# Optimization experiments

Measured on AMD Instinct MI355X. Metric: run time of the kernel, lower is better.

## Reference

```python
import math
import jax, jax.numpy as jnp
import numpy as np

B, T, C, HS = 8, 2048, 1024, 64

def setup_inputs() -> dict:
    key = jax.random.key(0)
    kx, kq, kk, kv = jax.random.split(key, 4)
    x = jax.random.normal(kx, (B, T, C), dtype=jnp.float32)
    # match nn.Linear init scale roughly: U(-1/sqrt(C), 1/sqrt(C))
    lim = 1.0 / math.sqrt(C)
    Wq = jax.random.uniform(kq, (C, HS), minval=-lim, maxval=lim, dtype=jnp.float32)
    Wk = jax.random.uniform(kk, (C, HS), minval=-lim, maxval=lim, dtype=jnp.float32)
    Wv = jax.random.uniform(kv, (C, HS), minval=-lim, maxval=lim, dtype=jnp.float32)
    return {"x": x, "Wq": Wq, "Wk": Wk, "Wv": Wv}

def reference(x, Wq, Wk, Wv):
    # NOTE: original scales by 1/sqrt(hs) where hs = x.shape[-1] = embd_size,
    # not head_size. Faithfully reproduced.
    Tlen = x.shape[1]
    scale = 1.0 / math.sqrt(x.shape[-1])
    q = jnp.einsum('btc,ch->bth', x, Wq)
    k = jnp.einsum('btc,ch->bth', x, Wk)
    v = jnp.einsum('btc,ch->bth', x, Wv)
    wei = jnp.einsum('bth,bsh->bts', q, k) * scale  # [B,T,T]
    causal = jnp.tril(jnp.ones((Tlen, Tlen), dtype=bool))
    wei = jnp.where(causal, wei, -jnp.inf)
    wei = jax.nn.softmax(wei, axis=-1)
    # dropout p=0.0 -> identity
    out = jnp.einsum('bts,bsh->bth', wei, v)  # [B,T,HS]
    return out
```

## Files before the change

kernel.cpp:

```cpp
#include <hip/hip_runtime.h>
#include <hip/hip_bf16.h>


#define T_SEQ 2048
#define C_DIM 1024
#define HS 64
#define BT 16384

typedef short s8v __attribute__((ext_vector_type(8)));
typedef float f4v __attribute__((ext_vector_type(4)));

__device__ inline unsigned short f2bf(float f) {
  union { float f; unsigned u; } a; a.f = f;
  unsigned r = a.u + 0x7fffu + ((a.u >> 16) & 1u);
  return (unsigned short)(r >> 16);
}

__device__ inline unsigned pk2(float a, float b) {
  union { __hip_bfloat162 h; unsigned u; } c;
  c.h = __float22bfloat162_rn(make_float2(a, b));
  return c.u;
}

__device__ inline s8v cvt8(float4 v0, float4 v1) {
  union { unsigned u[4]; s8v v; } r;
  r.u[0] = pk2(v0.x, v0.y); r.u[1] = pk2(v0.z, v0.w);
  r.u[2] = pk2(v1.x, v1.y); r.u[3] = pk2(v1.z, v1.w);
  return r.v;
}

__device__ inline void gl_lds16(const void* g, unsigned char* lds_base,
                                unsigned uniform_byte_off) {
  __builtin_amdgcn_global_load_lds(
      (const __attribute__((address_space(1))) unsigned int*)g,
      (__attribute__((address_space(3))) unsigned int*)(lds_base + uniform_byte_off),
      16, 0, 0);
}

__global__ __launch_bounds__(256) void wt_kernel(
    const float* __restrict__ Wq, const float* __restrict__ Wk,
    const float* __restrict__ Wv, unsigned short* __restrict__ wt) {
  __shared__ float tile[64][65];
  const int bid = blockIdx.x;
  const int mat = bid >> 4, kt = bid & 15;
  const float* W = (mat == 0) ? Wq : ((mat == 1) ? Wk : Wv);
  const int t = threadIdx.x;
  const int n = t & 63, kr = t >> 6;
#pragma unroll
  for (int j = 0; j < 16; ++j) {
    const int kl = j * 4 + kr;
    tile[kl][n] = W[(kt * 64 + kl) * HS + n];
  }
  __syncthreads();
  const int n2 = t >> 2, kp = t & 3;
  unsigned int* orow =
      (unsigned int*)(wt + (size_t)(mat * 64 + n2) * C_DIM + kt * 64);
#pragma unroll
  for (int i = 0; i < 8; ++i) {
    const int k0 = kp * 16 + i * 2;
    unsigned int lo = f2bf(tile[k0][n2]);
    unsigned int hi = f2bf(tile[k0 + 1][n2]);
    orow[kp * 8 + i] = lo | (hi << 16);
  }
}

__global__ __launch_bounds__(256) void qkv_kernel(
    const float* __restrict__ x, const unsigned short* __restrict__ wt,
    unsigned short* __restrict__ qws, unsigned short* __restrict__ kws,
    unsigned short* __restrict__ vtws) {
  __shared__ unsigned char abuf[2][8192];
  __shared__ unsigned char bbuf[2][24576];

  const int tid  = threadIdx.x;
  const int wv   = tid >> 6;
  const int lane = tid & 63;
  const int m    = lane & 15;
  const int quad = lane >> 4;
  const int row0 = blockIdx.x * 32;
  const int mh   = wv >> 1;
  const int ng   = (wv & 1) * 6;

  f4v acc[6];
#pragma unroll
  for (int j = 0; j < 6; ++j) acc[j] = (f4v)0.0f;

  const unsigned au = (unsigned)__builtin_amdgcn_readfirstlane(tid & 192) << 4;

  const float* agp[2];
#pragma unroll
  for (int j = 0; j < 2; ++j) {
    const int s = tid + j * 256;
    const int r = s >> 4, p = (s & 15) ^ (r & 15);
    agp[j] = x + (size_t)(row0 + r) * C_DIM + p * 4;
  }
  const unsigned short* bgp[6];
#pragma unroll
  for (int j = 0; j < 6; ++j) {
    const int s = tid + j * 256;
    const int n = s >> 3, p = (s & 7) ^ (n & 7);
    bgp[j] = wt + (size_t)n * C_DIM + p * 8;
  }

  int aoff[2][2];
#pragma unroll
  for (int c = 0; c < 2; ++c)
#pragma unroll
    for (int t = 0; t < 2; ++t)
      aoff[c][t] = (((mh * 16 + m) * 16) + ((c * 8 + 2 * quad + t) ^ m)) << 4;
  int boff[6][2];
#pragma unroll
  for (int j = 0; j < 6; ++j) {
    const int n = (ng + j) * 16 + m;
#pragma unroll
    for (int c = 0; c < 2; ++c)
      boff[j][c] = (n * 8 + ((c * 4 + quad) ^ (n & 7))) << 4;
  }

#define STAGE(buf, kk)                                                       \
  do {                                                                       \
    _Pragma("unroll") for (int j = 0; j < 2; ++j)                            \
        gl_lds16(agp[j] + (kk), abuf[buf], au + (unsigned)(j * 4096));       \
    _Pragma("unroll") for (int j = 0; j < 6; ++j)                            \
        gl_lds16(bgp[j] + (kk), bbuf[buf], au + (unsigned)(j * 4096));       \
  } while (0)

  STAGE(0, 0);
  for (int it = 0; it < 16; ++it) {
    __syncthreads();
    if (it < 15) STAGE((it + 1) & 1, (it + 1) * 64);
    const unsigned char* aB = abuf[it & 1];
    const unsigned char* bB = bbuf[it & 1];
#pragma unroll
    for (int c = 0; c < 2; ++c) {
      float4 xa = *(const float4*)(aB + aoff[c][0]);
      float4 xb = *(const float4*)(aB + aoff[c][1]);
      s8v a = cvt8(xa, xb);
#pragma unroll
      for (int j = 0; j < 6; ++j) {
        s8v b = *(const s8v*)(bB + boff[j][c]);
        acc[j] = __builtin_amdgcn_mfma_f32_16x16x32_bf16(a, b, acc[j], 0, 0, 0);
      }
    }
  }
#undef STAGE

  const float qscale = 1.4426950408889634f / 32.0f;
#pragma unroll
  for (int j = 0; j < 6; ++j) {
    const int nt = ng + j;
    const int mat = nt >> 2, ct = nt & 3;
    const int col = ct * 16 + m;
#pragma unroll
    for (int r = 0; r < 4; ++r) {
      const int row = row0 + mh * 16 + quad * 4 + r;
      const float v = acc[j][r];
      if (mat == 0) {
        qws[row * HS + col] = f2bf(v * qscale);
      } else if (mat == 1) {
        kws[row * HS + col] = f2bf(v);
      } else {
        const int bb = row >> 11, t = row & 2047;
        const int tp = (t & ~63) | (((t & 15) << 2) | ((t >> 4) & 3));
        vtws[(bb * HS + col) * T_SEQ + tp] = f2bf(v);
      }
    }
  }
}

union __align__(16) AttnSh {
  unsigned short p[8][2][16 * 72];
  float mo[8][32][64];
};

__global__ __launch_bounds__(512) void attn_kernel(
    const unsigned short* __restrict__ qws, const unsigned short* __restrict__ kws,
    const unsigned short* __restrict__ vtws, float* __restrict__ out) {
  __shared__ AttnSh sh;
  __shared__ float ml[8][32];

  const int tid  = threadIdx.x;
  const int wv   = tid >> 6;
  const int lane = tid & 63;
  const int m    = lane & 15;
  const int quad = lane >> 4;
  const int b    = blockIdx.x & 7;
  const int qi   = (T_SEQ / 32 - 1) - (blockIdx.x >> 3);
  const int r0   = qi * 32;
  const int gr0  = b * T_SEQ + r0;

  const unsigned short* qp = qws + (size_t)(gr0 + m) * HS + quad * 8;
  s8v aqA0 = *(const s8v*)qp;
  s8v aqA1 = *(const s8v*)(qp + 32);
  s8v aqB0 = *(const s8v*)(qp + 16 * HS);
  s8v aqB1 = *(const s8v*)(qp + 16 * HS + 32);

  float liA[4] = {0.f, 0.f, 0.f, 0.f};
  float liB[4] = {0.f, 0.f, 0.f, 0.f};
  f4v oA[4], oB[4];
#pragma unroll
  for (int i = 0; i < 4; ++i) { oA[i] = (f4v)0.0f; oB[i] = (f4v)0.0f; }

  const int nst = (r0 + 32 + 63) >> 6;
  unsigned short* plA = sh.p[wv][0];
  unsigned short* plB = sh.p[wv][1];
  const int qbA = r0 + quad * 4;
  const int qbB = qbA + 16;
  const unsigned short* kbase = kws + (size_t)b * T_SEQ * HS;
  const unsigned short* vbase = vtws + (size_t)b * HS * T_SEQ;

  for (int st = wv; st < nst; st += 8) {
    const int s0 = st * 64;

    s8v kf[4][2];
#pragma unroll
    for (int ns = 0; ns < 4; ++ns) {
      const unsigned short* kp = &kbase[(size_t)(s0 + ns * 16 + m) * HS + quad * 8];
      kf[ns][0] = *(const s8v*)kp;
      kf[ns][1] = *(const s8v*)(kp + 32);
    }
    s8v vf[4][2];
#pragma unroll
    for (int hn = 0; hn < 4; ++hn) {
      const unsigned short* vp = &vbase[(size_t)(hn * 16 + m) * T_SEQ + s0 + quad * 8];
      vf[hn][0] = *(const s8v*)vp;
      vf[hn][1] = *(const s8v*)(vp + 32);
    }

    f4v sa[4], sb[4];
#pragma unroll
    for (int ns = 0; ns < 4; ++ns) {
      f4v t = (f4v)0.0f;
      t = __builtin_amdgcn_mfma_f32_16x16x32_bf16(aqA0, kf[ns][0], t, 0, 0, 0);
      t = __builtin_amdgcn_mfma_f32_16x16x32_bf16(aqA1, kf[ns][1], t, 0, 0, 0);
      sa[ns] = t;
      f4v u = (f4v)0.0f;
      u = __builtin_amdgcn_mfma_f32_16x16x32_bf16(aqB0, kf[ns][0], u, 0, 0, 0);
      u = __builtin_amdgcn_mfma_f32_16x16x32_bf16(aqB1, kf[ns][1], u, 0, 0, 0);
      sb[ns] = u;
    }

    const int sm = s0 + m;
#pragma unroll
    for (int r = 0; r < 4; ++r) {
      const int qr = qbA + r;
      const float p0 = (sm      > qr) ? 0.f : __builtin_amdgcn_exp2f(sa[0][r]);
      const float p1 = (sm + 16 > qr) ? 0.f : __builtin_amdgcn_exp2f(sa[1][r]);
      const float p2 = (sm + 32 > qr) ? 0.f : __builtin_amdgcn_exp2f(sa[2][r]);
      const float p3 = (sm + 48 > qr) ? 0.f : __builtin_amdgcn_exp2f(sa[3][r]);
      liA[r] += (p0 + p1) + (p2 + p3);
      *(uint2*)&plA[(quad * 4 + r) * 72 + m * 4] =
          make_uint2(pk2(p0, p1), pk2(p2, p3));
    }
#pragma unroll
    for (int r = 0; r < 4; ++r) {
      const int qr = qbB + r;
      const float p0 = (sm      > qr) ? 0.f : __builtin_amdgcn_exp2f(sb[0][r]);
      const float p1 = (sm + 16 > qr) ? 0.f : __builtin_amdgcn_exp2f(sb[1][r]);
      const float p2 = (sm + 32 > qr) ? 0.f : __builtin_amdgcn_exp2f(sb[2][r]);
      const float p3 = (sm + 48 > qr) ? 0.f : __builtin_amdgcn_exp2f(sb[3][r]);
      liB[r] += (p0 + p1) + (p2 + p3);
      *(uint2*)&plB[(quad * 4 + r) * 72 + m * 4] =
          make_uint2(pk2(p0, p1), pk2(p2, p3));
    }

    s8v apA0 = *(const s8v*)&plA[m * 72 + quad * 8];
    s8v apA1 = *(const s8v*)&plA[m * 72 + 32 + quad * 8];
    s8v apB0 = *(const s8v*)&plB[m * 72 + quad * 8];
    s8v apB1 = *(const s8v*)&plB[m * 72 + 32 + quad * 8];
#pragma unroll
    for (int hn = 0; hn < 4; ++hn) {
      oA[hn] = __builtin_amdgcn_mfma_f32_16x16x32_bf16(apA0, vf[hn][0], oA[hn], 0, 0, 0);
      oA[hn] = __builtin_amdgcn_mfma_f32_16x16x32_bf16(apA1, vf[hn][1], oA[hn], 0, 0, 0);
      oB[hn] = __builtin_amdgcn_mfma_f32_16x16x32_bf16(apB0, vf[hn][0], oB[hn], 0, 0, 0);
      oB[hn] = __builtin_amdgcn_mfma_f32_16x16x32_bf16(apB1, vf[hn][1], oB[hn], 0, 0, 0);
    }
  }

#pragma unroll
  for (int r = 0; r < 4; ++r) {
    float s = liA[r];
    s += __shfl_xor(s, 1); s += __shfl_xor(s, 2);
    s += __shfl_xor(s, 4); s += __shfl_xor(s, 8);
    liA[r] = s;
    float u = liB[r];
    u += __shfl_xor(u, 1); u += __shfl_xor(u, 2);
    u += __shfl_xor(u, 4); u += __shfl_xor(u, 8);
    liB[r] = u;
  }

  __syncthreads();

#pragma unroll
  for (int hn = 0; hn < 4; ++hn)
#pragma unroll
    for (int r = 0; r < 4; ++r) {
      sh.mo[wv][quad * 4 + r][hn * 16 + m] = oA[hn][r];
      sh.mo[wv][16 + quad * 4 + r][hn * 16 + m] = oB[hn][r];
    }
  if (m == 0) {
#pragma unroll
    for (int r = 0; r < 4; ++r) {
      ml[wv][quad * 4 + r] = liA[r];
      ml[wv][16 + quad * 4 + r] = liB[r];
    }
  }
  __syncthreads();

  const int row = tid >> 4, c4 = (tid & 15) * 4;
  float ls = 0.f;
#pragma unroll
  for (int w = 0; w < 8; ++w) ls += ml[w][row];
  const float inv = 1.0f / ls;
  float ax = 0.f, ay = 0.f, az = 0.f, aw = 0.f;
#pragma unroll
  for (int w = 0; w < 8; ++w) {
    float4 v = *(const float4*)&sh.mo[w][row][c4];
    ax += v.x; ay += v.y; az += v.z; aw += v.w;
  }
  float4 res;
  res.x = ax * inv; res.y = ay * inv; res.z = az * inv; res.w = aw * inv;
  *(float4*)&out[(size_t)(gr0 + row) * HS + c4] = res;
}

extern "C" void kernel_launch(void* const* d_in, const int* in_sizes, int n_in,
                              void* d_out, int out_size, void* d_ws, size_t ws_size,
                              hipStream_t stream) {
  const float* x  = (const float*)d_in[0];
  const float* Wq = (const float*)d_in[1];
  const float* Wk = (const float*)d_in[2];
  const float* Wv = (const float*)d_in[3];
  float* out = (float*)d_out;

  unsigned short* qws  = (unsigned short*)d_ws;
  unsigned short* kws  = qws + (size_t)BT * HS;
  unsigned short* vtws = kws + (size_t)BT * HS;
  unsigned short* wt   = vtws + (size_t)BT * HS;

  wt_kernel<<<dim3(48), dim3(256), 0, stream>>>(Wq, Wk, Wv, wt);
  qkv_kernel<<<dim3(BT / 32), dim3(256), 0, stream>>>(x, wt, qws, kws, vtws);
  attn_kernel<<<dim3(512), dim3(512), 0, stream>>>(qws, kws, vtws, out);
}
```

Before: 137.7 us.

## Pair short and long causal query tiles per block to balance attention work

Each attention block now handles two 32-row query tiles, one near the start and one near the end of the sequence, so every block does roughly the same causal work. The grid shrinks from 512 to 256 blocks, and each K/V tile loaded from global memory is reused for up to four query sub-tiles. In exchange, register pressure rises from the 16 output accumulators per thread, only 256 blocks are launched, and the final reduction runs in two passes through shared memory.

Result: no change. 135.4 us (-1.6%).

```diff
diff --git a/kernel.cpp b/kernel.cpp
--- a/kernel.cpp
+++ b/kernel.cpp
@@ -168,7 +168,7 @@
 }
 
 union __align__(16) AttnSh {
-  unsigned short p[8][2][16 * 72];
+  unsigned short p[8][4][16 * 72];
   float mo[8][32][64];
 };
 
@@ -184,31 +184,73 @@
   const int m    = lane & 15;
   const int quad = lane >> 4;
   const int b    = blockIdx.x & 7;
-  const int qi   = (T_SEQ / 32 - 1) - (blockIdx.x >> 3);
-  const int r0   = qi * 32;
-  const int gr0  = b * T_SEQ + r0;
-
-  const unsigned short* qp = qws + (size_t)(gr0 + m) * HS + quad * 8;
-  s8v aqA0 = *(const s8v*)qp;
-  s8v aqA1 = *(const s8v*)(qp + 32);
-  s8v aqB0 = *(const s8v*)(qp + 16 * HS);
-  s8v aqB1 = *(const s8v*)(qp + 16 * HS + 32);
-
-  float liA[4] = {0.f, 0.f, 0.f, 0.f};
-  float liB[4] = {0.f, 0.f, 0.f, 0.f};
-  f4v oA[4], oB[4];
-#pragma unroll
-  for (int i = 0; i < 4; ++i) { oA[i] = (f4v)0.0f; oB[i] = (f4v)0.0f; }
-
-  const int nst = (r0 + 32 + 63) >> 6;
-  unsigned short* plA = sh.p[wv][0];
-  unsigned short* plB = sh.p[wv][1];
-  const int qbA = r0 + quad * 4;
-  const int qbB = qbA + 16;
+  const int pr   = blockIdx.x >> 3;
+  const int rS   = pr * 32;
+  const int rB   = (63 - pr) * 32;
+  const int grS  = b * T_SEQ + rS;
+  const int grB  = b * T_SEQ + rB;
+
+  const unsigned short* qpS = qws + (size_t)(grS + m) * HS + quad * 8;
+  const unsigned short* qpB = qws + (size_t)(grB + m) * HS + quad * 8;
+  s8v aq[4][2];
+  aq[0][0] = *(const s8v*)qpS;
+  aq[0][1] = *(const s8v*)(qpS + 32);
+  aq[1][0] = *(const s8v*)(qpS + 16 * HS);
+  aq[1][1] = *(const s8v*)(qpS + 16 * HS + 32);
+  aq[2][0] = *(const s8v*)qpB;
+  aq[2][1] = *(const s8v*)(qpB + 32);
+  aq[3][0] = *(const s8v*)(qpB + 16 * HS);
+  aq[3][1] = *(const s8v*)(qpB + 16 * HS + 32);
+
+  float li[4][4];
+  f4v o[4][4];
+#pragma unroll
+  for (int t = 0; t < 4; ++t)
+#pragma unroll
+    for (int i = 0; i < 4; ++i) { li[t][i] = 0.f; o[t][i] = (f4v)0.0f; }
+
+  const int nstS = (rS + 32 + 63) >> 6;
+  const int nstB = (rB + 32 + 63) >> 6;
+  const int qb0 = rS + quad * 4;
+  const int qb1 = qb0 + 16;
+  const int qb2 = rB + quad * 4;
+  const int qb3 = qb2 + 16;
   const unsigned short* kbase = kws + (size_t)b * T_SEQ * HS;
   const unsigned short* vbase = vtws + (size_t)b * HS * T_SEQ;
 
-  for (int st = wv; st < nst; st += 8) {
+#define QKT(t, qbase)                                                        \
+  {                                                                          \
+    f4v s_[4];                                                               \
+    _Pragma("unroll") for (int ns = 0; ns < 4; ++ns) {                       \
+      f4v u_ = (f4v)0.0f;                                                    \
+      u_ = __builtin_amdgcn_mfma_f32_16x16x32_bf16(aq[t][0], kf[ns][0], u_, 0, 0, 0); \
+      u_ = __builtin_amdgcn_mfma_f32_16x16x32_bf16(aq[t][1], kf[ns][1], u_, 0, 0, 0); \
+      s_[ns] = u_;                                                           \
+    }                                                                        \
+    _Pragma("unroll") for (int r = 0; r < 4; ++r) {                          \
+      const int qr = (qbase) + r;                                            \
+      const float p0 = (sm      > qr) ? 0.f : __builtin_amdgcn_exp2f(s_[0][r]); \
+      const float p1 = (sm + 16 > qr) ? 0.f : __builtin_amdgcn_exp2f(s_[1][r]); \
+      const float p2 = (sm + 32 > qr) ? 0.f : __builtin_amdgcn_exp2f(s_[2][r]); \
+      const float p3 = (sm + 48 > qr) ? 0.f : __builtin_amdgcn_exp2f(s_[3][r]); \
+      li[t][r] += (p0 + p1) + (p2 + p3);                                     \
+      *(uint2*)&sh.p[wv][t][(quad * 4 + r) * 72 + m * 4] =                   \
+          make_uint2(pk2(p0, p1), pk2(p2, p3));                              \
+    }                                                                        \
+  }
+
+#define PVT(t)                                                               \
+  {                                                                          \
+    const unsigned short* pl_ = sh.p[wv][t];                                 \
+    s8v a0_ = *(const s8v*)&pl_[m * 72 + quad * 8];                          \
+    s8v a1_ = *(const s8v*)&pl_[m * 72 + 32 + quad * 8];                     \
+    _Pragma("unroll") for (int hn = 0; hn < 4; ++hn) {                       \
+      o[t][hn] = __builtin_amdgcn_mfma_f32_16x16x32_bf16(a0_, vf[hn][0], o[t][hn], 0, 0, 0); \
+      o[t][hn] = __builtin_amdgcn_mfma_f32_16x16x32_bf16(a1_, vf[hn][1], o[t][hn], 0, 0, 0); \
+    }                                                                        \
+  }
+
+  for (int st = wv; st < nstB; st += 8) {
     const int s0 = st * 64;
 
     s8v kf[4][2];
@@ -226,100 +268,63 @@
       vf[hn][1] = *(const s8v*)(vp + 32);
     }
 
-    f4v sa[4], sb[4];
-#pragma unroll
-    for (int ns = 0; ns < 4; ++ns) {
-      f4v t = (f4v)0.0f;
-      t = __builtin_amdgcn_mfma_f32_16x16x32_bf16(aqA0, kf[ns][0], t, 0, 0, 0);
-      t = __builtin_amdgcn_mfma_f32_16x16x32_bf16(aqA1, kf[ns][1], t, 0, 0, 0);
-      sa[ns] = t;
-      f4v u = (f4v)0.0f;
-      u = __builtin_amdgcn_mfma_f32_16x16x32_bf16(aqB0, kf[ns][0], u, 0, 0, 0);
-      u = __builtin_amdgcn_mfma_f32_16x16x32_bf16(aqB1, kf[ns][1], u, 0, 0, 0);
-      sb[ns] = u;
-    }
-
     const int sm = s0 + m;
+    const bool low = (st < nstS);
+    if (low) { QKT(0, qb0); QKT(1, qb1); }
+    QKT(2, qb2);
+    QKT(3, qb3);
+    if (low) { PVT(0); PVT(1); }
+    PVT(2);
+    PVT(3);
+  }
+#undef QKT
+#undef PVT
+
+#pragma unroll
+  for (int t = 0; t < 4; ++t)
 #pragma unroll
     for (int r = 0; r < 4; ++r) {
-      const int qr = qbA + r;
-      const float p0 = (sm      > qr) ? 0.f : __builtin_amdgcn_exp2f(sa[0][r]);
-      const float p1 = (sm + 16 > qr) ? 0.f : __builtin_amdgcn_exp2f(sa[1][r]);
-      const float p2 = (sm + 32 > qr) ? 0.f : __builtin_amdgcn_exp2f(sa[2][r]);
-      const float p3 = (sm + 48 > qr) ? 0.f : __builtin_amdgcn_exp2f(sa[3][r]);
-      liA[r] += (p0 + p1) + (p2 + p3);
-      *(uint2*)&plA[(quad * 4 + r) * 72 + m * 4] =
-          make_uint2(pk2(p0, p1), pk2(p2, p3));
-    }
-#pragma unroll
-    for (int r = 0; r < 4; ++r) {
-      const int qr = qbB + r;
-      const float p0 = (sm      > qr) ? 0.f : __builtin_amdgcn_exp2f(sb[0][r]);
-      const float p1 = (sm + 16 > qr) ? 0.f : __builtin_amdgcn_exp2f(sb[1][r]);
-      const float p2 = (sm + 32 > qr) ? 0.f : __builtin_amdgcn_exp2f(sb[2][r]);
-      const float p3 = (sm + 48 > qr) ? 0.f : __builtin_amdgcn_exp2f(sb[3][r]);
-      liB[r] += (p0 + p1) + (p2 + p3);
-      *(uint2*)&plB[(quad * 4 + r) * 72 + m * 4] =
-          make_uint2(pk2(p0, p1), pk2(p2, p3));
-    }
-
-    s8v apA0 = *(const s8v*)&plA[m * 72 + quad * 8];
-    s8v apA1 = *(const s8v*)&plA[m * 72 + 32 + quad * 8];
-    s8v apB0 = *(const s8v*)&plB[m * 72 + quad * 8];
-    s8v apB1 = *(const s8v*)&plB[m * 72 + 32 + quad * 8];
-#pragma unroll
-    for (int hn = 0; hn < 4; ++hn) {
-      oA[hn] = __builtin_amdgcn_mfma_f32_16x16x32_bf16(apA0, vf[hn][0], oA[hn], 0, 0, 0);
-      oA[hn] = __builtin_amdgcn_mfma_f32_16x16x32_bf16(apA1, vf[hn][1], oA[hn], 0, 0, 0);
-      oB[hn] = __builtin_amdgcn_mfma_f32_16x16x32_bf16(apB0, vf[hn][0], oB[hn], 0, 0, 0);
-      oB[hn] = __builtin_amdgcn_mfma_f32_16x16x32_bf16(apB1, vf[hn][1], oB[hn], 0, 0, 0);
-    }
-  }
-
-#pragma unroll
-  for (int r = 0; r < 4; ++r) {
-    float s = liA[r];
-    s += __shfl_xor(s, 1); s += __shfl_xor(s, 2);
-    s += __shfl_xor(s, 4); s += __shfl_xor(s, 8);
-    liA[r] = s;
-    float u = liB[r];
-    u += __shfl_xor(u, 1); u += __shfl_xor(u, 2);
-    u += __shfl_xor(u, 4); u += __shfl_xor(u, 8);
-    liB[r] = u;
-  }
-
-  __syncthreads();
-
-#pragma unroll
-  for (int hn = 0; hn < 4; ++hn)
-#pragma unroll
-    for (int r = 0; r < 4; ++r) {
-      sh.mo[wv][quad * 4 + r][hn * 16 + m] = oA[hn][r];
-      sh.mo[wv][16 + quad * 4 + r][hn * 16 + m] = oB[hn][r];
-    }
-  if (m == 0) {
-#pragma unroll
-    for (int r = 0; r < 4; ++r) {
-      ml[wv][quad * 4 + r] = liA[r];
-      ml[wv][16 + quad * 4 + r] = liB[r];
-    }
-  }
-  __syncthreads();
+      float s = li[t][r];
+      s += __shfl_xor(s, 1); s += __shfl_xor(s, 2);
+      s += __shfl_xor(s, 4); s += __shfl_xor(s, 8);
+      li[t][r] = s;
+    }
 
   const int row = tid >> 4, c4 = (tid & 15) * 4;
-  float ls = 0.f;
-#pragma unroll
-  for (int w = 0; w < 8; ++w) ls += ml[w][row];
-  const float inv = 1.0f / ls;
-  float ax = 0.f, ay = 0.f, az = 0.f, aw = 0.f;
-#pragma unroll
-  for (int w = 0; w < 8; ++w) {
-    float4 v = *(const float4*)&sh.mo[w][row][c4];
-    ax += v.x; ay += v.y; az += v.z; aw += v.w;
-  }
-  float4 res;
-  res.x = ax * inv; res.y = ay * inv; res.z = az * inv; res.w = aw * inv;
-  *(float4*)&out[(size_t)(gr0 + row) * HS + c4] = res;
+#pragma unroll
+  for (int ps = 0; ps < 2; ++ps) {
+    __syncthreads();
+#pragma unroll
+    for (int hn = 0; hn < 4; ++hn)
+#pragma unroll
+      for (int r = 0; r < 4; ++r) {
+        sh.mo[wv][quad * 4 + r][hn * 16 + m]      = o[2 * ps][hn][r];
+        sh.mo[wv][16 + quad * 4 + r][hn * 16 + m] = o[2 * ps + 1][hn][r];
+      }
+    if (m == 0) {
+#pragma unroll
+      for (int r = 0; r < 4; ++r) {
+        ml[wv][quad * 4 + r]      = li[2 * ps][r];
+        ml[wv][16 + quad * 4 + r] = li[2 * ps + 1][r];
+      }
+    }
+    __syncthreads();
+
+    float ls = 0.f;
+#pragma unroll
+    for (int w = 0; w < 8; ++w) ls += ml[w][row];
+    const float inv = 1.0f / ls;
+    float ax = 0.f, ay = 0.f, az = 0.f, aw = 0.f;
+#pragma unroll
+    for (int w = 0; w < 8; ++w) {
+      float4 v = *(const float4*)&sh.mo[w][row][c4];
+      ax += v.x; ay += v.y; az += v.z; aw += v.w;
+    }
+    const int gr = ps ? grB : grS;
+    float4 res;
+    res.x = ax * inv; res.y = ay * inv; res.z = az * inv; res.w = aw * inv;
+    *(float4*)&out[(size_t)(gr + row) * HS + c4] = res;
+  }
 }
 
 extern "C" void kernel_launch(void* const* d_in, const int* in_sizes, int n_in,
@@ -338,5 +343,5 @@
 
   wt_kernel<<<dim3(48), dim3(256), 0, stream>>>(Wq, Wk, Wv, wt);
   qkv_kernel<<<dim3(BT / 32), dim3(256), 0, stream>>>(x, wt, qws, kws, vtws);
-  attn_kernel<<<dim3(512), dim3(512), 0, stream>>>(qws, kws, vtws, out);
-}
+  attn_kernel<<<dim3(256), dim3(512), 0, stream>>>(qws, kws, vtws, out);
+}
```
